# Optimization experiments

Hardware: AMD Instinct MI355X
Metric: run time of the kernel (lower is better)

The kernel has to match this reference:

```python
import jax, jax.numpy as jnp
import numpy as np

N = 50000   # nodes
E = 800000  # edges
IN_DIM = 512
HID = 256   # total hidden (4 heads x 64)
HEADS = 4
OUT_DIM = 256
NEG_SLOPE = 0.2


def setup_inputs() -> dict:
    key = jax.random.key(0)
    ks = jax.random.split(key, 16)
    s = 0.05
    d = {
        "feats": jax.random.normal(ks[0], (N, IN_DIM), jnp.float32),
        "src": jax.random.randint(ks[1], (E,), 0, N, jnp.int32),
        "dst": jax.random.randint(ks[2], (E,), 0, N, jnp.int32),
        # layer 0: in 512 -> 4 heads x 64
        "W0": jax.random.normal(ks[3], (IN_DIM, HID), jnp.float32) * s,
        "al0": jax.random.normal(ks[4], (HEADS, HID // HEADS), jnp.float32) * s,
        "ar0": jax.random.normal(ks[5], (HEADS, HID // HEADS), jnp.float32) * s,
        "b0": jnp.zeros((HID,), jnp.float32),
        # layer 1: in 256 -> 4 heads x 64
        "W1": jax.random.normal(ks[6], (HID, HID), jnp.float32) * s,
        "al1": jax.random.normal(ks[7], (HEADS, HID // HEADS), jnp.float32) * s,
        "ar1": jax.random.normal(ks[8], (HEADS, HID // HEADS), jnp.float32) * s,
        "b1": jnp.zeros((HID,), jnp.float32),
        # layer 2: in 256 -> 1 head x 256, no activation
        "W2": jax.random.normal(ks[9], (HID, OUT_DIM), jnp.float32) * s,
        "al2": jax.random.normal(ks[10], (1, OUT_DIM), jnp.float32) * s,
        "ar2": jax.random.normal(ks[11], (1, OUT_DIM), jnp.float32) * s,
        "b2": jnp.zeros((OUT_DIM,), jnp.float32),
    }
    return d


def gat_conv(h, src, dst, W, al, ar, b, act):
    """DGL-style GATConv (no dropout, no residual). Returns [N, H, D]."""
    H, D = al.shape
    feat = (h @ W).reshape(-1, H, D)                       # [N,H,D]
    el = jnp.einsum('nhd,hd->nh', feat, al)                # [N,H]
    er = jnp.einsum('nhd,hd->nh', feat, ar)                # [N,H]
    e = jax.nn.leaky_relu(el[src] + er[dst], NEG_SLOPE)    # [E,H]
    # edge softmax over incoming edges per destination node
    m = jax.ops.segment_max(e, dst, num_segments=N)        # [N,H]
    ex = jnp.exp(e - m[dst])                               # [E,H]
    s = jax.ops.segment_sum(ex, dst, num_segments=N)       # [N,H]
    alpha = ex / s[dst]                                    # [E,H]
    msg = jax.ops.segment_sum(alpha[:, :, None] * feat[src], dst, num_segments=N)  # [N,H,D]
    out = msg + b.reshape(1, H, D)
    return act(out) if act is not None else out


def reference(feats, src, dst, W0, al0, ar0, b0, W1, al1, ar1, b1, W2, al2, ar2, b2):
    h = gat_conv(feats, src, dst, W0, al0, ar0, b0, jax.nn.relu)
    h = h.reshape(h.shape[0], -1)                          # flatten heads
    h = gat_conv(h, src, dst, W1, al1, ar1, b1, jax.nn.relu)
    h = h.reshape(h.shape[0], -1)
    h = gat_conv(h, src, dst, W2, al2, ar2, b2, None)
    h = h.mean(axis=1)                                     # last layer: mean over (single) head
    return h
```

## Files before the change

### kernel.cpp

```cpp
#include <hip/hip_runtime.h>
#include <hip/hip_bf16.h>
#include <math.h>


#define HID 256

typedef __attribute__((ext_vector_type(8))) __bf16 bf16x8;
typedef __attribute__((ext_vector_type(4))) __bf16 bf16x4;
typedef __attribute__((ext_vector_type(8))) _Float16 half8;
typedef __attribute__((ext_vector_type(4))) _Float16 half4;
typedef __attribute__((ext_vector_type(4))) float floatx4;

__device__ __forceinline__ void gl_lds16(const void* g, void* l) {
    __builtin_amdgcn_global_load_lds(
        (const __attribute__((address_space(1))) void*)g,
        (__attribute__((address_space(3))) void*)l, 16, 0, 0);
}


__global__ void hist_kernel(const int* __restrict__ dst, int* __restrict__ cnt, int E) {
    int e = blockIdx.x * blockDim.x + threadIdx.x;
    if (e < E) atomicAdd(&cnt[dst[e]], 1);
}

__global__ __launch_bounds__(256) void scan1_kernel(const int* __restrict__ cnt,
                                                    int* __restrict__ bsum, int n) {
    __shared__ int w[4];
    int t = threadIdx.x;
    int i = blockIdx.x * 256 + t;
    int c = (i < n) ? cnt[i] : 0;
    int acc = c;
#pragma unroll
    for (int off = 32; off > 0; off >>= 1) acc += __shfl_xor(acc, off);
    if ((t & 63) == 0) w[t >> 6] = acc;
    __syncthreads();
    if (t == 0) bsum[blockIdx.x] = w[0] + w[1] + w[2] + w[3];
}

__global__ __launch_bounds__(256) void scan2_kernel(const int* __restrict__ bsum,
                                                    int* __restrict__ boff, int nb) {
    __shared__ int buf[256];
    int t = threadIdx.x;
    int v = (t < nb) ? bsum[t] : 0;
    buf[t] = v;
    __syncthreads();
    for (int off = 1; off < 256; off <<= 1) {
        int x = (t >= off) ? buf[t - off] : 0;
        __syncthreads();
        buf[t] += x;
        __syncthreads();
    }
    if (t < nb) boff[t] = buf[t] - v;
}

__global__ __launch_bounds__(256) void scan3_kernel(const int* __restrict__ cnt,
                                                    const int* __restrict__ boff,
                                                    int* __restrict__ rowptr,
                                                    int* __restrict__ cursor, int n) {
    __shared__ int buf[256];
    int t = threadIdx.x;
    int i = blockIdx.x * 256 + t;
    int c = (i < n) ? cnt[i] : 0;
    buf[t] = c;
    __syncthreads();
    for (int off = 1; off < 256; off <<= 1) {
        int x = (t >= off) ? buf[t - off] : 0;
        __syncthreads();
        buf[t] += x;
        __syncthreads();
    }
    int start = boff[blockIdx.x] + buf[t] - c;
    if (i < n) {
        rowptr[i] = start;
        cursor[i] = start;
        if (i == n - 1) rowptr[n] = start + c;
    }
}

__global__ void fill_kernel(const int* __restrict__ src, const int* __restrict__ dst,
                            int* __restrict__ cursor, int* __restrict__ adj, int E) {
    int e = blockIdx.x * blockDim.x + threadIdx.x;
    if (e < E) {
        int d = dst[e];
        int pos = atomicAdd(&cursor[d], 1);
        adj[pos] = src[e];
    }
}


__device__ __forceinline__ void splitT_one(const float* W, __bf16* ht, __bf16* lt,
                                           int idx, int K) {
    int k = idx >> 8, n = idx & 255;
    float v = W[idx];
    __bf16 h = (__bf16)v;
    ht[(size_t)n * K + k] = h;
    lt[(size_t)n * K + k] = (__bf16)(v - (float)h);
}

__global__ __launch_bounds__(256) void splitT_all_kernel(
    const float* __restrict__ W0, const float* __restrict__ W1,
    const float* __restrict__ W2, __bf16* h0, __bf16* l0, __bf16* h1,
    __bf16* l1, __bf16* h2, __bf16* l2) {
    int i = blockIdx.x * 256 + threadIdx.x;
    const int n0 = 512 * 256, n1 = 256 * 256;
    if (i < n0) splitT_one(W0, h0, l0, i, 512);
    else if (i < n0 + n1) splitT_one(W1, h1, l1, i - n0, 256);
    else if (i < n0 + 2 * n1) splitT_one(W2, h2, l2, i - n0 - n1, 256);
}


template <bool SPLITA>
__global__ __launch_bounds__(256, 2) void gemm_mfma_kernel(
    const float* __restrict__ Af, const __bf16* __restrict__ Ah,
    const __bf16* __restrict__ Al, const __bf16* __restrict__ Bht,
    const __bf16* __restrict__ Blt, _Float16* __restrict__ C,
    const float* __restrict__ al, const float* __restrict__ ar,
    float* __restrict__ el, float* __restrict__ er, int M, int K, int H) {
    __shared__ __bf16 sAh[128 * 32];
    __shared__ __bf16 sAl[128 * 32];
    __shared__ __bf16 sBh[128 * 32];
    __shared__ __bf16 sBl[128 * 32];

    int t = threadIdx.x;
    int wave = t >> 6, lane = t & 63;
    int wr = wave >> 1, wc = wave & 1;
    int quad = lane >> 4, m16 = lane & 15;

    int rowA0 = blockIdx.y * 128;
    int rowB0 = blockIdx.x * 128;

    int sr = t >> 2;
    int ke = (t & 3) * 8;
    int ldso = t * 8;
    int srow = t >> 1;
    int kb = (t & 1) * 16;

    size_t ar0 = 0, ar1 = 0, af0 = 0;
    if (SPLITA) {
        af0 = (size_t)min(rowA0 + srow, M - 1) * K + kb;
    } else {
        ar0 = (size_t)min(rowA0 + sr, M - 1) * K;
        ar1 = (size_t)min(rowA0 + sr + 64, M - 1) * K;
    }
    size_t br0 = (size_t)(rowB0 + sr) * K;
    size_t br1 = (size_t)(rowB0 + sr + 64) * K;

    floatx4 acc[4][4];
    floatx4 z = {0.f, 0.f, 0.f, 0.f};
#pragma unroll
    for (int i = 0; i < 4; i++)
#pragma unroll
        for (int j = 0; j < 4; j++) acc[i][j] = z;

    int nk = K >> 5;
    for (int kt = 0; kt < nk; kt++) {
        int k0s = (kt << 5) + ke;
        gl_lds16(Bht + br0 + k0s, &sBh[ldso]);
        gl_lds16(Bht + br1 + k0s, &sBh[2048 + ldso]);
        gl_lds16(Blt + br0 + k0s, &sBl[ldso]);
        gl_lds16(Blt + br1 + k0s, &sBl[2048 + ldso]);
        if (SPLITA) {
            const float* ap = Af + af0 + (kt << 5);
            float4 v0 = ((const float4*)ap)[0];
            float4 v1 = ((const float4*)ap)[1];
            float4 v2 = ((const float4*)ap)[2];
            float4 v3 = ((const float4*)ap)[3];
            float vv[16] = {v0.x, v0.y, v0.z, v0.w, v1.x, v1.y, v1.z, v1.w,
                            v2.x, v2.y, v2.z, v2.w, v3.x, v3.y, v3.z, v3.w};
            bf16x8 h0, h1, l0, l1;
#pragma unroll
            for (int c = 0; c < 8; c++) {
                __bf16 hv = (__bf16)vv[c];
                h0[c] = hv;
                l0[c] = (__bf16)(vv[c] - (float)hv);
                __bf16 hv2 = (__bf16)vv[8 + c];
                h1[c] = hv2;
                l1[c] = (__bf16)(vv[8 + c] - (float)hv2);
            }
            int so = srow * 32 + kb;
            *(bf16x8*)&sAh[so] = h0;
            *(bf16x8*)&sAh[so + 8] = h1;
            *(bf16x8*)&sAl[so] = l0;
            *(bf16x8*)&sAl[so + 8] = l1;
        } else {
            gl_lds16(Ah + ar0 + k0s, &sAh[ldso]);
            gl_lds16(Ah + ar1 + k0s, &sAh[2048 + ldso]);
            gl_lds16(Al + ar0 + k0s, &sAl[ldso]);
            gl_lds16(Al + ar1 + k0s, &sAl[2048 + ldso]);
        }
        __syncthreads();

        bf16x8 fah[4], fal[4], fbh[4], fbl[4];
#pragma unroll
        for (int i = 0; i < 4; i++) {
            int off = (wr * 64 + i * 16 + m16) * 32 + quad * 8;
            fah[i] = *(const bf16x8*)&sAh[off];
            fal[i] = *(const bf16x8*)&sAl[off];
        }
#pragma unroll
        for (int j = 0; j < 4; j++) {
            int off = (wc * 64 + j * 16 + m16) * 32 + quad * 8;
            fbh[j] = *(const bf16x8*)&sBh[off];
            fbl[j] = *(const bf16x8*)&sBl[off];
        }
#pragma unroll
        for (int i = 0; i < 4; i++)
#pragma unroll
            for (int j = 0; j < 4; j++) {
                acc[i][j] = __builtin_amdgcn_mfma_f32_16x16x32_bf16(fah[i], fbh[j], acc[i][j], 0, 0, 0);
                acc[i][j] = __builtin_amdgcn_mfma_f32_16x16x32_bf16(fah[i], fbl[j], acc[i][j], 0, 0, 0);
                acc[i][j] = __builtin_amdgcn_mfma_f32_16x16x32_bf16(fal[i], fbh[j], acc[i][j], 0, 0, 0);
            }
        __syncthreads();
    }

#pragma unroll
    for (int i = 0; i < 4; i++) {
        int rowb = rowA0 + wr * 64 + i * 16 + quad * 4;
#pragma unroll
        for (int j = 0; j < 4; j++) {
            int col = rowB0 + wc * 64 + j * 16 + m16;
#pragma unroll
            for (int r = 0; r < 4; r++) {
                int row = rowb + r;
                if (row < M) C[(size_t)row * HID + col] = (_Float16)acc[i][j][r];
            }
        }
    }

    float alv[4], arv[4];
#pragma unroll
    for (int j = 0; j < 4; j++) {
        int col = rowB0 + wc * 64 + j * 16 + m16;
        alv[j] = al[col];
        arv[j] = ar[col];
    }
    int h = ((rowB0 + wc * 64) >> 6) & (H - 1);
#pragma unroll
    for (int i = 0; i < 4; i++) {
        int rowb = rowA0 + wr * 64 + i * 16 + quad * 4;
#pragma unroll
        for (int r = 0; r < 4; r++) {
            float pe = acc[i][0][r] * alv[0] + acc[i][1][r] * alv[1] +
                       acc[i][2][r] * alv[2] + acc[i][3][r] * alv[3];
            float pr = acc[i][0][r] * arv[0] + acc[i][1][r] * arv[1] +
                       acc[i][2][r] * arv[2] + acc[i][3][r] * arv[3];
#pragma unroll
            for (int off = 1; off < 16; off <<= 1) {
                pe += __shfl_xor(pe, off);
                pr += __shfl_xor(pr, off);
            }
            int row = rowb + r;
            if (m16 == 0 && row < M) {
                if (H == 4) {
                    el[row * 4 + h] = pe;
                    er[row * 4 + h] = pr;
                } else {
                    atomicAdd(&el[row], pe);
                    atomicAdd(&er[row], pr);
                }
            }
        }
    }
}


__global__ __launch_bounds__(256) void gemm_kernel(const float* __restrict__ A,
                                                   const float* __restrict__ B,
                                                   _Float16* __restrict__ C,
                                                   int M, int K, int Nn) {
    __shared__ float As[16][128];
    __shared__ float Bs[16][128];

    int t = threadIdx.x;
    int tx = t & 15, ty = t >> 4;
    int arow = t >> 1;
    int acol = (t & 1) * 8;
    int brow = t >> 4;
    int bcol = (t & 15) * 8;

    int gArow = blockIdx.y * 128 + arow;
    const float* aPtr = A + (size_t)gArow * K + acol;
    const float* bPtr = B + (size_t)brow * Nn + blockIdx.x * 128 + bcol;

    float acc[8][8];
#pragma unroll
    for (int i = 0; i < 8; i++)
#pragma unroll
        for (int j = 0; j < 8; j++) acc[i][j] = 0.f;

    bool aok = (gArow < M);
    int nk = K >> 4;
    for (int kt = 0; kt < nk; kt++) {
        int k0 = kt << 4;
        float4 av0 = make_float4(0.f, 0.f, 0.f, 0.f), av1 = av0;
        if (aok) {
            av0 = *(const float4*)(aPtr + k0);
            av1 = *(const float4*)(aPtr + k0 + 4);
        }
        float4 bv0 = *(const float4*)(bPtr + (size_t)k0 * Nn);
        float4 bv1 = *(const float4*)(bPtr + (size_t)k0 * Nn + 4);

        As[acol + 0][arow] = av0.x;
        As[acol + 1][arow] = av0.y;
        As[acol + 2][arow] = av0.z;
        As[acol + 3][arow] = av0.w;
        As[acol + 4][arow] = av1.x;
        As[acol + 5][arow] = av1.y;
        As[acol + 6][arow] = av1.z;
        As[acol + 7][arow] = av1.w;
        *(float4*)&Bs[brow][bcol] = bv0;
        *(float4*)&Bs[brow][bcol + 4] = bv1;
        __syncthreads();

#pragma unroll
        for (int kk = 0; kk < 16; kk++) {
            float4 a0 = *(const float4*)&As[kk][ty * 4];
            float4 a1 = *(const float4*)&As[kk][64 + ty * 4];
            float4 b0 = *(const float4*)&Bs[kk][tx * 4];
            float4 b1 = *(const float4*)&Bs[kk][64 + tx * 4];
            float a[8] = {a0.x, a0.y, a0.z, a0.w, a1.x, a1.y, a1.z, a1.w};
            float b[8] = {b0.x, b0.y, b0.z, b0.w, b1.x, b1.y, b1.z, b1.w};
#pragma unroll
            for (int i = 0; i < 8; i++)
#pragma unroll
                for (int j = 0; j < 8; j++) acc[i][j] = fmaf(a[i], b[j], acc[i][j]);
        }
        __syncthreads();
    }

    int c0 = blockIdx.x * 128 + tx * 4;
#pragma unroll
    for (int half = 0; half < 2; half++) {
#pragma unroll
        for (int i = 0; i < 4; i++) {
            int r = blockIdx.y * 128 + half * 64 + ty * 4 + i;
            if (r < M) {
                _Float16* cp = C + (size_t)r * Nn + c0;
                int ai = half * 4 + i;
#pragma unroll
                for (int j = 0; j < 4; j++) {
                    cp[j] = (_Float16)acc[ai][j];
                    cp[64 + j] = (_Float16)acc[ai][4 + j];
                }
            }
        }
    }
}


__global__ __launch_bounds__(256) void elr_kernel(const _Float16* __restrict__ feat,
                                                  const float* __restrict__ al,
                                                  const float* __restrict__ ar,
                                                  float* __restrict__ el,
                                                  float* __restrict__ er, int H) {
    int n = blockIdx.x, t = threadIdx.x;
    float f = (float)feat[(size_t)n * HID + t];
    float a = f * al[t];
    float b = f * ar[t];
#pragma unroll
    for (int off = 32; off > 0; off >>= 1) {
        a += __shfl_xor(a, off);
        b += __shfl_xor(b, off);
    }
    __shared__ float pa[4], pb[4];
    int wave = t >> 6, lane = t & 63;
    if (lane == 0) { pa[wave] = a; pb[wave] = b; }
    __syncthreads();
    if (H == 4) {
        if (t < 4) {
            el[n * 4 + t] = pa[t];
            er[n * 4 + t] = pb[t];
        }
    } else {
        if (t == 0) {
            el[n] = pa[0] + pa[1] + pa[2] + pa[3];
            er[n] = pb[0] + pb[1] + pb[2] + pb[3];
        }
    }
}


template <int H, bool RELU, bool WF32, bool WSPLIT>
__global__ __launch_bounds__(256) void agg_tpl(
    const _Float16* __restrict__ feat, const float* __restrict__ el,
    const float* __restrict__ er, const int* __restrict__ rowptr,
    const int* __restrict__ adj, const float* __restrict__ bias,
    _Float16* __restrict__ exbuf,
    float* __restrict__ outf, __bf16* __restrict__ oh, __bf16* __restrict__ ol,
    int N) {
    int wave = threadIdx.x >> 6, lane = threadIdx.x & 63;
    int v = blockIdx.x * 4 + wave;
    if (v >= N) return;
    int row0 = rowptr[v];
    int deg = rowptr[v + 1] - row0;

    int l32 = lane & 31;
    int half = lane >> 5;
    int hd = (H == 4) ? (l32 >> 3) : 0;
    int d0 = l32 * 8;

    float o[8];
    if (deg > 0) {
        float s[H], er_v[H];
#pragma unroll
        for (int h = 0; h < H; h++) {
            er_v[h] = er[v * H + h];
            s[h] = 0.f;
        }

        for (int e = lane; e < deg; e += 64) {
            int u = adj[row0 + e];
            if (H == 4) {
                float4 elu = *(const float4*)&el[u * 4];
                float ev[4] = {elu.x, elu.y, elu.z, elu.w};
                half4 exq;
#pragma unroll
                for (int h = 0; h < 4; h++) {
                    float sc = ev[h] + er_v[h];
                    sc = (sc > 0.f) ? sc : 0.2f * sc;
                    float ex = __expf(sc);
                    s[h] += ex;
                    exq[h] = (_Float16)ex;
                }
                *(half4*)&exbuf[(size_t)(row0 + e) * 4] = exq;
            } else {
                float sc = el[u] + er_v[0];
                sc = (sc > 0.f) ? sc : 0.2f * sc;
                float ex = __expf(sc);
                s[0] += ex;
                exbuf[row0 + e] = (_Float16)ex;
            }
        }
#pragma unroll
        for (int h = 0; h < H; h++)
#pragma unroll
            for (int off = 32; off > 0; off >>= 1) s[h] += __shfl_xor(s[h], off);

        __threadfence_block();

        float s_l = (H == 4) ? ((l32 & 16) ? ((l32 & 8) ? s[3] : s[2])
                                           : ((l32 & 8) ? s[1] : s[0]))
                             : s[0];
        float inv_l = 1.f / s_l;

        const _Float16* exb = exbuf + (size_t)row0 * H;
        const int* adjr = adj + row0;

        float a[8];
#pragma unroll
        for (int j = 0; j < 8; j++) a[j] = 0.f;

        int e = 0;
        for (; e + 16 <= deg; e += 16) {
            int u[8];
            float alp[8];
            half8 f[8];
#pragma unroll
            for (int q = 0; q < 8; q++) {
                int ee = e + q * 2 + half;
                u[q] = adjr[ee];
                alp[q] = (float)exb[ee * H + hd];
            }
#pragma unroll
            for (int q = 0; q < 8; q++)
                f[q] = *(const half8*)&feat[(size_t)u[q] * HID + d0];
#pragma unroll
            for (int q = 0; q < 8; q++) {
                float al_ = alp[q] * inv_l;
#pragma unroll
                for (int j = 0; j < 8; j++) a[j] = fmaf(al_, (float)f[q][j], a[j]);
            }
        }
        for (; e + 8 <= deg; e += 8) {
            int u[4];
            float alp[4];
            half8 f[4];
#pragma unroll
            for (int q = 0; q < 4; q++) {
                int ee = e + q * 2 + half;
                u[q] = adjr[ee];
                alp[q] = (float)exb[ee * H + hd];
            }
#pragma unroll
            for (int q = 0; q < 4; q++)
                f[q] = *(const half8*)&feat[(size_t)u[q] * HID + d0];
#pragma unroll
            for (int q = 0; q < 4; q++) {
                float al_ = alp[q] * inv_l;
#pragma unroll
                for (int j = 0; j < 8; j++) a[j] = fmaf(al_, (float)f[q][j], a[j]);
            }
        }
        for (; e < deg; e += 2) {
            int ee = e + half;
            bool act = ee < deg;
            int es = act ? ee : (deg - 1);
            int u = adjr[es];
            float al_ = act ? ((float)exb[es * H + hd] * inv_l) : 0.f;
            half8 f = *(const half8*)&feat[(size_t)u * HID + d0];
#pragma unroll
            for (int j = 0; j < 8; j++) a[j] = fmaf(al_, (float)f[j], a[j]);
        }
#pragma unroll
        for (int j = 0; j < 8; j++) a[j] += __shfl_xor(a[j], 32);

#pragma unroll
        for (int j = 0; j < 8; j++) {
            o[j] = a[j] + bias[d0 + j];
            if (RELU) o[j] = fmaxf(o[j], 0.f);
        }
    } else {
#pragma unroll
        for (int j = 0; j < 8; j++) {
            o[j] = bias[d0 + j];
            if (RELU) o[j] = fmaxf(o[j], 0.f);
        }
    }

    if (half == 0) {
        size_t base = (size_t)v * HID + d0;
        if (WF32) {
            *(float4*)&outf[base] = make_float4(o[0], o[1], o[2], o[3]);
            *(float4*)&outf[base + 4] = make_float4(o[4], o[5], o[6], o[7]);
        }
        if (WSPLIT) {
            bf16x8 hh, ll;
#pragma unroll
            for (int j = 0; j < 8; j++) {
                __bf16 hv = (__bf16)o[j];
                hh[j] = hv;
                ll[j] = (__bf16)(o[j] - (float)hv);
            }
            *(bf16x8*)&oh[base] = hh;
            *(bf16x8*)&ol[base] = ll;
        }
    }
}


extern "C" void kernel_launch(void* const* d_in, const int* in_sizes, int n_in,
                              void* d_out, int out_size, void* d_ws, size_t ws_size,
                              hipStream_t stream) {
    const float* feats = (const float*)d_in[0];
    const int* src = (const int*)d_in[1];
    const int* dst = (const int*)d_in[2];
    const float* W0 = (const float*)d_in[3];
    const float* al0 = (const float*)d_in[4];
    const float* ar0 = (const float*)d_in[5];
    const float* b0 = (const float*)d_in[6];
    const float* W1 = (const float*)d_in[7];
    const float* al1 = (const float*)d_in[8];
    const float* ar1 = (const float*)d_in[9];
    const float* b1 = (const float*)d_in[10];
    const float* W2 = (const float*)d_in[11];
    const float* al2 = (const float*)d_in[12];
    const float* ar2 = (const float*)d_in[13];
    const float* b2 = (const float*)d_in[14];
    float* out = (float*)d_out;

    const int IN_DIM = 512;
    const int N = in_sizes[0] / IN_DIM;
    const int E = in_sizes[1];

    char* ws = (char*)d_ws;
    size_t off = 0;
    auto alloc = [&](size_t bytes) -> void* {
        void* p = ws + off;
        off = (off + bytes + 255) & ~(size_t)255;
        return p;
    };
    _Float16* featbuf = (_Float16*)alloc((size_t)N * HID * sizeof(_Float16));
    float* el = (float*)alloc((size_t)N * 4 * sizeof(float));
    float* er = (float*)alloc((size_t)N * 4 * sizeof(float));
    int* cnt = (int*)alloc((size_t)N * sizeof(int));
    int* rowptr = (int*)alloc((size_t)(N + 1) * sizeof(int));
    int* cursor = (int*)alloc((size_t)N * sizeof(int));
    int* adj = (int*)alloc((size_t)E * sizeof(int));
    _Float16* exbuf = (_Float16*)alloc((size_t)E * 4 * sizeof(_Float16));
    int nscanb = (N + 255) / 256;
    int* bsum = (int*)alloc((size_t)nscanb * sizeof(int));
    int* boff = (int*)alloc((size_t)nscanb * sizeof(int));
    __bf16* Ah = (__bf16*)alloc((size_t)N * HID * sizeof(__bf16));
    __bf16* Al = (__bf16*)alloc((size_t)N * HID * sizeof(__bf16));
    __bf16* Bht0 = (__bf16*)alloc((size_t)512 * HID * sizeof(__bf16));
    __bf16* Blt0 = (__bf16*)alloc((size_t)512 * HID * sizeof(__bf16));
    __bf16* Bht1 = (__bf16*)alloc((size_t)256 * HID * sizeof(__bf16));
    __bf16* Blt1 = (__bf16*)alloc((size_t)256 * HID * sizeof(__bf16));
    __bf16* Bht2 = (__bf16*)alloc((size_t)256 * HID * sizeof(__bf16));
    __bf16* Blt2 = (__bf16*)alloc((size_t)256 * HID * sizeof(__bf16));
    bool use_mfma = (off <= ws_size);

    hipMemsetAsync(cnt, 0, (size_t)N * sizeof(int), stream);
    hist_kernel<<<(E + 255) / 256, 256, 0, stream>>>(dst, cnt, E);
    scan1_kernel<<<nscanb, 256, 0, stream>>>(cnt, bsum, N);
    scan2_kernel<<<1, 256, 0, stream>>>(bsum, boff, nscanb);
    scan3_kernel<<<nscanb, 256, 0, stream>>>(cnt, boff, rowptr, cursor, N);
    fill_kernel<<<(E + 255) / 256, 256, 0, stream>>>(src, dst, cursor, adj, E);

    dim3 ggrid(HID / 128, (N + 127) / 128);
    int aggb = (N + 3) / 4;

    if (use_mfma) {
        splitT_all_kernel<<<(512 * 256 + 2 * 256 * 256) / 256, 256, 0, stream>>>(
            W0, W1, W2, Bht0, Blt0, Bht1, Blt1, Bht2, Blt2);

        gemm_mfma_kernel<true><<<ggrid, 256, 0, stream>>>(
            feats, nullptr, nullptr, Bht0, Blt0, featbuf, al0, ar0, el, er, N, 512, 4);
        agg_tpl<4, true, false, true><<<aggb, 256, 0, stream>>>(
            featbuf, el, er, rowptr, adj, b0, exbuf, nullptr, Ah, Al, N);

        gemm_mfma_kernel<false><<<ggrid, 256, 0, stream>>>(
            nullptr, Ah, Al, Bht1, Blt1, featbuf, al1, ar1, el, er, N, 256, 4);
        agg_tpl<4, true, false, true><<<aggb, 256, 0, stream>>>(
            featbuf, el, er, rowptr, adj, b1, exbuf, nullptr, Ah, Al, N);

        hipMemsetAsync(el, 0, (size_t)N * 8 * sizeof(float), stream);
        gemm_mfma_kernel<false><<<ggrid, 256, 0, stream>>>(
            nullptr, Ah, Al, Bht2, Blt2, featbuf, al2, ar2, el, er, N, 256, 1);
        agg_tpl<1, false, true, false><<<aggb, 256, 0, stream>>>(
            featbuf, el, er, rowptr, adj, b2, exbuf, out, nullptr, nullptr, N);
    } else {
        gemm_kernel<<<ggrid, 256, 0, stream>>>(feats, W0, featbuf, N, 512, HID);
        elr_kernel<<<N, 256, 0, stream>>>(featbuf, al0, ar0, el, er, 4);
        agg_tpl<4, true, true, false><<<aggb, 256, 0, stream>>>(
            featbuf, el, er, rowptr, adj, b0, exbuf, out, nullptr, nullptr, N);

        gemm_kernel<<<ggrid, 256, 0, stream>>>(out, W1, featbuf, N, 256, HID);
        elr_kernel<<<N, 256, 0, stream>>>(featbuf, al1, ar1, el, er, 4);
        agg_tpl<4, true, true, false><<<aggb, 256, 0, stream>>>(
            featbuf, el, er, rowptr, adj, b1, exbuf, out, nullptr, nullptr, N);

        gemm_kernel<<<ggrid, 256, 0, stream>>>(out, W2, featbuf, N, 256, HID);
        elr_kernel<<<N, 256, 0, stream>>>(featbuf, al2, ar2, el, er, 1);
        agg_tpl<1, false, true, false><<<aggb, 256, 0, stream>>>(
            featbuf, el, er, rowptr, adj, b2, exbuf, out, nullptr, nullptr, N);
    }
}
```

Measured before the change: 640.4 us.

## Fuse edge softmax into aggregation loop, dropping exbuf pass and normalization

The aggregation kernel no longer makes a separate pass over incoming edges to compute exp scores into an fp16 edge buffer and sum them. Each lane now computes the leaky-relu/exp score inline as it gathers neighbour features, accumulates the unnormalised weighted sum and the denominator together, and divides once at the end. This removes the exbuf writes and reads and one wave reduction per node, at the cost of recomputing exp per half-wave lane (once per head-lane rather than once per edge). Like the old code it does not subtract the segment max, so very large scores could overflow.

```diff
diff --git a/kernel.cpp b/kernel.cpp
--- a/kernel.cpp
+++ b/kernel.cpp
@@ -386,7 +386,6 @@
     const _Float16* __restrict__ feat, const float* __restrict__ el,
     const float* __restrict__ er, const int* __restrict__ rowptr,
     const int* __restrict__ adj, const float* __restrict__ bias,
-    _Float16* __restrict__ exbuf,
     float* __restrict__ outf, __bf16* __restrict__ oh, __bf16* __restrict__ ol,
     int N) {
     int wave = threadIdx.x >> 6, lane = threadIdx.x & 63;
@@ -402,94 +401,57 @@
 
     float o[8];
     if (deg > 0) {
-        float s[H], er_v[H];
-#pragma unroll
-        for (int h = 0; h < H; h++) {
-            er_v[h] = er[v * H + h];
-            s[h] = 0.f;
-        }
-
-        for (int e = lane; e < deg; e += 64) {
-            int u = adj[row0 + e];
-            if (H == 4) {
-                float4 elu = *(const float4*)&el[u * 4];
-                float ev[4] = {elu.x, elu.y, elu.z, elu.w};
-                half4 exq;
-#pragma unroll
-                for (int h = 0; h < 4; h++) {
-                    float sc = ev[h] + er_v[h];
-                    sc = (sc > 0.f) ? sc : 0.2f * sc;
-                    float ex = __expf(sc);
-                    s[h] += ex;
-                    exq[h] = (_Float16)ex;
-                }
-                *(half4*)&exbuf[(size_t)(row0 + e) * 4] = exq;
-            } else {
-                float sc = el[u] + er_v[0];
-                sc = (sc > 0.f) ? sc : 0.2f * sc;
-                float ex = __expf(sc);
-                s[0] += ex;
-                exbuf[row0 + e] = (_Float16)ex;
-            }
-        }
-#pragma unroll
-        for (int h = 0; h < H; h++)
-#pragma unroll
-            for (int off = 32; off > 0; off >>= 1) s[h] += __shfl_xor(s[h], off);
-
-        __threadfence_block();
-
-        float s_l = (H == 4) ? ((l32 & 16) ? ((l32 & 8) ? s[3] : s[2])
-                                           : ((l32 & 8) ? s[1] : s[0]))
-                             : s[0];
-        float inv_l = 1.f / s_l;
-
-        const _Float16* exb = exbuf + (size_t)row0 * H;
+        float er_h = (H == 4) ? er[v * 4 + hd] : er[v];
         const int* adjr = adj + row0;
 
         float a[8];
 #pragma unroll
         for (int j = 0; j < 8; j++) a[j] = 0.f;
+        float sl = 0.f;
 
         int e = 0;
         for (; e + 16 <= deg; e += 16) {
             int u[8];
-            float alp[8];
             half8 f[8];
-#pragma unroll
-            for (int q = 0; q < 8; q++) {
-                int ee = e + q * 2 + half;
-                u[q] = adjr[ee];
-                alp[q] = (float)exb[ee * H + hd];
-            }
+            float elv[8];
+#pragma unroll
+            for (int q = 0; q < 8; q++) u[q] = adjr[e + q * 2 + half];
 #pragma unroll
             for (int q = 0; q < 8; q++)
                 f[q] = *(const half8*)&feat[(size_t)u[q] * HID + d0];
 #pragma unroll
+            for (int q = 0; q < 8; q++)
+                elv[q] = (H == 4) ? el[u[q] * 4 + hd] : el[u[q]];
+#pragma unroll
             for (int q = 0; q < 8; q++) {
-                float al_ = alp[q] * inv_l;
-#pragma unroll
-                for (int j = 0; j < 8; j++) a[j] = fmaf(al_, (float)f[q][j], a[j]);
+                float sc = elv[q] + er_h;
+                sc = (sc > 0.f) ? sc : 0.2f * sc;
+                float ex = __expf(sc);
+                sl += ex;
+#pragma unroll
+                for (int j = 0; j < 8; j++) a[j] = fmaf(ex, (float)f[q][j], a[j]);
             }
         }
         for (; e + 8 <= deg; e += 8) {
             int u[4];
-            float alp[4];
             half8 f[4];
-#pragma unroll
-            for (int q = 0; q < 4; q++) {
-                int ee = e + q * 2 + half;
-                u[q] = adjr[ee];
-                alp[q] = (float)exb[ee * H + hd];
-            }
+            float elv[4];
+#pragma unroll
+            for (int q = 0; q < 4; q++) u[q] = adjr[e + q * 2 + half];
 #pragma unroll
             for (int q = 0; q < 4; q++)
                 f[q] = *(const half8*)&feat[(size_t)u[q] * HID + d0];
 #pragma unroll
+            for (int q = 0; q < 4; q++)
+                elv[q] = (H == 4) ? el[u[q] * 4 + hd] : el[u[q]];
+#pragma unroll
             for (int q = 0; q < 4; q++) {
-                float al_ = alp[q] * inv_l;
-#pragma unroll
-                for (int j = 0; j < 8; j++) a[j] = fmaf(al_, (float)f[q][j], a[j]);
+                float sc = elv[q] + er_h;
+                sc = (sc > 0.f) ? sc : 0.2f * sc;
+                float ex = __expf(sc);
+                sl += ex;
+#pragma unroll
+                for (int j = 0; j < 8; j++) a[j] = fmaf(ex, (float)f[q][j], a[j]);
             }
         }
         for (; e < deg; e += 2) {
@@ -497,17 +459,24 @@
             bool act = ee < deg;
             int es = act ? ee : (deg - 1);
             int u = adjr[es];
-            float al_ = act ? ((float)exb[es * H + hd] * inv_l) : 0.f;
+            float elvq = (H == 4) ? el[u * 4 + hd] : el[u];
             half8 f = *(const half8*)&feat[(size_t)u * HID + d0];
-#pragma unroll
-            for (int j = 0; j < 8; j++) a[j] = fmaf(al_, (float)f[j], a[j]);
-        }
+            float sc = elvq + er_h;
+            sc = (sc > 0.f) ? sc : 0.2f * sc;
+            float ex = act ? __expf(sc) : 0.f;
+            sl += ex;
+#pragma unroll
+            for (int j = 0; j < 8; j++) a[j] = fmaf(ex, (float)f[j], a[j]);
+        }
+
 #pragma unroll
         for (int j = 0; j < 8; j++) a[j] += __shfl_xor(a[j], 32);
+        sl += __shfl_xor(sl, 32);
+        float inv = 1.f / sl;
 
 #pragma unroll
         for (int j = 0; j < 8; j++) {
-            o[j] = a[j] + bias[d0 + j];
+            o[j] = fmaf(a[j], inv, bias[d0 + j]);
             if (RELU) o[j] = fmaxf(o[j], 0.f);
         }
     } else {
@@ -577,7 +546,6 @@
     int* rowptr = (int*)alloc((size_t)(N + 1) * sizeof(int));
     int* cursor = (int*)alloc((size_t)N * sizeof(int));
     int* adj = (int*)alloc((size_t)E * sizeof(int));
-    _Float16* exbuf = (_Float16*)alloc((size_t)E * 4 * sizeof(_Float16));
     int nscanb = (N + 255) / 256;
     int* bsum = (int*)alloc((size_t)nscanb * sizeof(int));
     int* boff = (int*)alloc((size_t)nscanb * sizeof(int));
@@ -608,32 +576,32 @@
         gemm_mfma_kernel<true><<<ggrid, 256, 0, stream>>>(
             feats, nullptr, nullptr, Bht0, Blt0, featbuf, al0, ar0, el, er, N, 512, 4);
         agg_tpl<4, true, false, true><<<aggb, 256, 0, stream>>>(
-            featbuf, el, er, rowptr, adj, b0, exbuf, nullptr, Ah, Al, N);
+            featbuf, el, er, rowptr, adj, b0, nullptr, Ah, Al, N);
 
         gemm_mfma_kernel<false><<<ggrid, 256, 0, stream>>>(
             nullptr, Ah, Al, Bht1, Blt1, featbuf, al1, ar1, el, er, N, 256, 4);
         agg_tpl<4, true, false, true><<<aggb, 256, 0, stream>>>(
-            featbuf, el, er, rowptr, adj, b1, exbuf, nullptr, Ah, Al, N);
+            featbuf, el, er, rowptr, adj, b1, nullptr, Ah, Al, N);
 
         hipMemsetAsync(el, 0, (size_t)N * 8 * sizeof(float), stream);
         gemm_mfma_kernel<false><<<ggrid, 256, 0, stream>>>(
             nullptr, Ah, Al, Bht2, Blt2, featbuf, al2, ar2, el, er, N, 256, 1);
         agg_tpl<1, false, true, false><<<aggb, 256, 0, stream>>>(
-            featbuf, el, er, rowptr, adj, b2, exbuf, out, nullptr, nullptr, N);
+            featbuf, el, er, rowptr, adj, b2, out, nullptr, nullptr, N);
     } else {
         gemm_kernel<<<ggrid, 256, 0, stream>>>(feats, W0, featbuf, N, 512, HID);
         elr_kernel<<<N, 256, 0, stream>>>(featbuf, al0, ar0, el, er, 4);
         agg_tpl<4, true, true, false><<<aggb, 256, 0, stream>>>(
-            featbuf, el, er, rowptr, adj, b0, exbuf, out, nullptr, nullptr, N);
+            featbuf, el, er, rowptr, adj, b0, out, nullptr, nullptr, N);
 
         gemm_kernel<<<ggrid, 256, 0, stream>>>(out, W1, featbuf, N, 256, HID);
         elr_kernel<<<N, 256, 0, stream>>>(featbuf, al1, ar1, el, er, 4);
         agg_tpl<4, true, true, false><<<aggb, 256, 0, stream>>>(
-            featbuf, el, er, rowptr, adj, b1, exbuf, out, nullptr, nullptr, N);
+            featbuf, el, er, rowptr, adj, b1, out, nullptr, nullptr, N);
 
         gemm_kernel<<<ggrid, 256, 0, stream>>>(out, W2, featbuf, N, 256, HID);
         elr_kernel<<<N, 256, 0, stream>>>(featbuf, al2, ar2, el, er, 1);
         agg_tpl<1, false, true, false><<<aggb, 256, 0, stream>>>(
-            featbuf, el, er, rowptr, adj, b2, exbuf, out, nullptr, nullptr, N);
-    }
-}
+            featbuf, el, er, rowptr, adj, b2, out, nullptr, nullptr, N);
+    }
+}
```

After: 614.3 us. -4.1%, faster.
